# Kernel optimization log

Hardware: AMD Instinct MI355X
Metric: run time of the kernel (lower is better)

## Reference

```python
import jax, jax.numpy as jnp
import numpy as np

EPS_RMS = 1e-6
EPS_Q = 1e-5


def _weight_quant(w):
    # BitNet b1.58-style ternary weight quantization with mean-abs scale
    scale = 1.0 / jnp.clip(jnp.mean(jnp.abs(w)), EPS_Q)
    wq = jnp.clip(jnp.round(w * scale), -1.0, 1.0) / scale
    return w + jax.lax.stop_gradient(wq - w)  # STE


def _activation_quant(x):
    # per-token 8-bit absmax quantization
    scale = 127.0 / jnp.clip(jnp.max(jnp.abs(x), axis=-1, keepdims=True), EPS_Q)
    xq = jnp.clip(jnp.round(x * scale), -128.0, 127.0) / scale
    return x + jax.lax.stop_gradient(xq - x)  # STE


def _rmsnorm(x, weight):
    inv = jax.lax.rsqrt(jnp.mean(x * x, axis=-1, keepdims=True) + EPS_RMS)
    return x * inv * weight


def setup_inputs() -> dict:
    key = jax.random.key(0)
    k1, k2, k3 = jax.random.split(key, 3)
    B, S, D, CD = 8, 4096, 1024, 1024
    x = jax.random.normal(k1, (B, S, D), dtype=jnp.float32)
    c = jax.random.normal(k2, (B, CD), dtype=jnp.float32)
    # NOTE: the module zero-inits proj; we use small random weights so the
    # quantized conditioning path is numerically exercised.
    w_proj = jax.random.normal(k3, (2 * D, CD), dtype=jnp.float32) * 0.02
    b_proj = jnp.zeros((2 * D,), dtype=jnp.float32)
    rms_weight = jnp.ones((D,), dtype=jnp.float32)
    return {"x": x, "c": c, "w_proj": w_proj, "b_proj": b_proj, "rms_weight": rms_weight}


def reference(x, c, w_proj, b_proj, rms_weight):
    if c.ndim == 2:
        c = c[:, None, :]  # [B, 1, cond_dim]
    # BitLinear: quantized activations x quantized ternary weights
    cq = _activation_quant(c)
    wq = _weight_quant(w_proj)
    emb = jnp.einsum('btc,dc->btd', cq, wq) + b_proj  # [B, 1, 2*dim]
    scale, shift = jnp.split(emb, 2, axis=-1)
    xn = _rmsnorm(x, rms_weight)
    return xn * (1.0 + scale) + shift
```

## Files before the change

### kernel.cpp

```cpp
#include <hip/hip_runtime.h>
#include <math.h>


constexpr int Bn = 8;
constexpr int Sn = 4096;
constexpr int Dn = 1024;
constexpr int TWO_D = 2048;
constexpr int OFF_PART = 0;
constexpr int OFF_CQ   = 4096;
constexpr int OFF_SC   = 16384;
constexpr int OFF_SH   = 24576;

__device__ __forceinline__ float waveReduceSumBcast(float v) {
#pragma unroll
    for (int off = 32; off > 0; off >>= 1) v += __shfl_xor(v, off, 64);
    return v;
}
__device__ __forceinline__ float waveReduceMaxBcast(float v) {
#pragma unroll
    for (int off = 32; off > 0; off >>= 1) v = fmaxf(v, __shfl_xor(v, off, 64));
    return v;
}

__global__ void k_pre(const float* __restrict__ w, const float* __restrict__ c,
                      float* __restrict__ part, float* __restrict__ cq) {
    int tid = threadIdx.x;
    if (blockIdx.x < TWO_D) {
        size_t base = (size_t)blockIdx.x * 1024 + (size_t)tid * 4;
        float4 v = *(const float4*)(w + base);
        float s = fabsf(v.x) + fabsf(v.y) + fabsf(v.z) + fabsf(v.w);
        s = waveReduceSumBcast(s);
        __shared__ float lds[4];
        if ((tid & 63) == 0) lds[tid >> 6] = s;
        __syncthreads();
        if (tid == 0) part[blockIdx.x] = lds[0] + lds[1] + lds[2] + lds[3];
    } else {
        int b = blockIdx.x - TWO_D;
        float4 v = ((const float4*)(c + (size_t)b * Dn))[tid];
        float m = fmaxf(fmaxf(fabsf(v.x), fabsf(v.y)), fmaxf(fabsf(v.z), fabsf(v.w)));
        m = waveReduceMaxBcast(m);
        __shared__ float lm[4];
        if ((tid & 63) == 0) lm[tid >> 6] = m;
        __syncthreads();
        float mx = fmaxf(fmaxf(lm[0], lm[1]), fmaxf(lm[2], lm[3]));
        float scale = 127.0f / fmaxf(mx, 1e-5f);
        float inv = 1.0f / scale;
        float4 q;
        q.x = fminf(fmaxf(rintf(v.x * scale), -128.0f), 127.0f) * inv;
        q.y = fminf(fmaxf(rintf(v.y * scale), -128.0f), 127.0f) * inv;
        q.z = fminf(fmaxf(rintf(v.z * scale), -128.0f), 127.0f) * inv;
        q.w = fminf(fmaxf(rintf(v.w * scale), -128.0f), 127.0f) * inv;
        ((float4*)(cq + (size_t)b * Dn))[tid] = q;
    }
}

__global__ void k_emb(const float* __restrict__ w, const float* __restrict__ bp,
                      const float* __restrict__ cq, const float* __restrict__ part,
                      float* __restrict__ sc, float* __restrict__ sh) {
    int tid = threadIdx.x;
    float s = 0.0f;
#pragma unroll
    for (int k = 0; k < 8; ++k) s += part[tid + k * 256];
    s = waveReduceSumBcast(s);
    __shared__ float lds[4];
    if ((tid & 63) == 0) lds[tid >> 6] = s;
    __syncthreads();
    float mw = fmaxf((lds[0] + lds[1] + lds[2] + lds[3]) * (1.0f / 2097152.0f), 1e-5f);
    float sw = 1.0f / mw;

    int lane = tid & 63;
    int d = (blockIdx.x * blockDim.x + tid) >> 6;
    const float* wr = w + (size_t)d * 1024 + (size_t)lane * 16;
    float t[16];
#pragma unroll
    for (int j = 0; j < 16; j += 4) {
        float4 v = *(const float4*)(wr + j);
        t[j + 0] = fminf(fmaxf(rintf(v.x * sw), -1.0f), 1.0f);
        t[j + 1] = fminf(fmaxf(rintf(v.y * sw), -1.0f), 1.0f);
        t[j + 2] = fminf(fmaxf(rintf(v.z * sw), -1.0f), 1.0f);
        t[j + 3] = fminf(fmaxf(rintf(v.w * sw), -1.0f), 1.0f);
    }
    for (int b = 0; b < Bn; ++b) {
        const float* cr = cq + (size_t)b * 1024 + (size_t)lane * 16;
        float dot = 0.0f;
#pragma unroll
        for (int j = 0; j < 16; j += 4) {
            float4 u = *(const float4*)(cr + j);
            dot += t[j + 0] * u.x + t[j + 1] * u.y + t[j + 2] * u.z + t[j + 3] * u.w;
        }
        dot = waveReduceSumBcast(dot);
        if (lane == 0) {
            float val = dot * mw + bp[d];
            if (d < Dn) sc[b * Dn + d] = 1.0f + val;
            else        sh[b * Dn + (d - Dn)] = val;
        }
    }
}

__global__ void __launch_bounds__(256) k_main(
        const float* __restrict__ x, const float* __restrict__ rw,
        const float* __restrict__ sc, const float* __restrict__ sh,
        float* __restrict__ out) {
    int tid  = threadIdx.x;
    int lane = tid & 63;
    int row  = blockIdx.x * 4 + (tid >> 6);
    int b    = row >> 12;

    const float4* xr = (const float4*)(x + (size_t)row * Dn);
    float4 v0 = xr[lane];
    float4 v1 = xr[lane + 64];
    float4 v2 = xr[lane + 128];
    float4 v3 = xr[lane + 192];

    float ss = v0.x*v0.x + v0.y*v0.y + v0.z*v0.z + v0.w*v0.w
             + v1.x*v1.x + v1.y*v1.y + v1.z*v1.z + v1.w*v1.w
             + v2.x*v2.x + v2.y*v2.y + v2.z*v2.z + v2.w*v2.w
             + v3.x*v3.x + v3.y*v3.y + v3.z*v3.z + v3.w*v3.w;
    ss = waveReduceSumBcast(ss);
    float inv = rsqrtf(ss * (1.0f / 1024.0f) + 1e-6f);

    const float4* rwv = (const float4*)rw;
    const float4* s1v = (const float4*)(sc + (size_t)b * Dn);
    const float4* s0v = (const float4*)(sh + (size_t)b * Dn);
    float4* ov = (float4*)(out + (size_t)row * Dn);

#pragma unroll
    for (int q = 0; q < 4; ++q) {
        int idx = lane + q * 64;
        float4 v = (q == 0) ? v0 : (q == 1) ? v1 : (q == 2) ? v2 : v3;
        float4 wv = rwv[idx];
        float4 s1 = s1v[idx];
        float4 s0 = s0v[idx];
        float4 o;
        o.x = v.x * inv * wv.x * s1.x + s0.x;
        o.y = v.y * inv * wv.y * s1.y + s0.y;
        o.z = v.z * inv * wv.z * s1.z + s0.z;
        o.w = v.w * inv * wv.w * s1.w + s0.w;
        ov[idx] = o;
    }
}

extern "C" void kernel_launch(void* const* d_in, const int* in_sizes, int n_in,
                              void* d_out, int out_size, void* d_ws, size_t ws_size,
                              hipStream_t stream) {
    const float* x  = (const float*)d_in[0];
    const float* c  = (const float*)d_in[1];
    const float* w  = (const float*)d_in[2];
    const float* bp = (const float*)d_in[3];
    const float* rw = (const float*)d_in[4];
    float* out = (float*)d_out;
    float* ws  = (float*)d_ws;

    float* part = ws + OFF_PART;
    float* cq   = ws + OFF_CQ;
    float* sc   = ws + OFF_SC;
    float* sh   = ws + OFF_SH;

    k_pre <<<TWO_D + Bn, 256, 0, stream>>>(w, c, part, cq);
    k_emb <<<TWO_D / 4, 256, 0, stream>>>(w, bp, cq, part, sc, sh);
    k_main<<<Bn * Sn / 4, 256, 0, stream>>>(x, rw, sc, sh, out);
}
```

Before: 63.30 us.

## Fold RMS weight into scale, prefetch rows with nontemporal loads in main kernel

Precomputes g = rms_weight*(1+scale) in the embedding kernel so the main kernel reads one fewer vector per element. The main kernel now launches fewer blocks, each processing four rows with the next row's data prefetched via nontemporal loads to overlap memory latency. The embedding kernel also batches wave reductions across all batches. Fewer blocks may reduce occupancy-based latency hiding.

```diff
diff --git a/kernel.cpp b/kernel.cpp
--- a/kernel.cpp
+++ b/kernel.cpp
@@ -8,8 +8,10 @@
 constexpr int TWO_D = 2048;
 constexpr int OFF_PART = 0;
 constexpr int OFF_CQ   = 4096;
-constexpr int OFF_SC   = 16384;
+constexpr int OFF_G    = 16384;
 constexpr int OFF_SH   = 24576;
+
+using f4 = __attribute__((ext_vector_type(4))) float;
 
 __device__ __forceinline__ float waveReduceSumBcast(float v) {
 #pragma unroll
@@ -27,7 +29,7 @@
     int tid = threadIdx.x;
     if (blockIdx.x < TWO_D) {
         size_t base = (size_t)blockIdx.x * 1024 + (size_t)tid * 4;
-        float4 v = *(const float4*)(w + base);
+        f4 v = *(const f4*)(w + base);
         float s = fabsf(v.x) + fabsf(v.y) + fabsf(v.z) + fabsf(v.w);
         s = waveReduceSumBcast(s);
         __shared__ float lds[4];
@@ -36,7 +38,7 @@
         if (tid == 0) part[blockIdx.x] = lds[0] + lds[1] + lds[2] + lds[3];
     } else {
         int b = blockIdx.x - TWO_D;
-        float4 v = ((const float4*)(c + (size_t)b * Dn))[tid];
+        f4 v = ((const f4*)(c + (size_t)b * Dn))[tid];
         float m = fmaxf(fmaxf(fabsf(v.x), fabsf(v.y)), fmaxf(fabsf(v.z), fabsf(v.w)));
         m = waveReduceMaxBcast(m);
         __shared__ float lm[4];
@@ -45,18 +47,19 @@
         float mx = fmaxf(fmaxf(lm[0], lm[1]), fmaxf(lm[2], lm[3]));
         float scale = 127.0f / fmaxf(mx, 1e-5f);
         float inv = 1.0f / scale;
-        float4 q;
+        f4 q;
         q.x = fminf(fmaxf(rintf(v.x * scale), -128.0f), 127.0f) * inv;
         q.y = fminf(fmaxf(rintf(v.y * scale), -128.0f), 127.0f) * inv;
         q.z = fminf(fmaxf(rintf(v.z * scale), -128.0f), 127.0f) * inv;
         q.w = fminf(fmaxf(rintf(v.w * scale), -128.0f), 127.0f) * inv;
-        ((float4*)(cq + (size_t)b * Dn))[tid] = q;
+        ((f4*)(cq + (size_t)b * Dn))[tid] = q;
     }
 }
 
 __global__ void k_emb(const float* __restrict__ w, const float* __restrict__ bp,
                       const float* __restrict__ cq, const float* __restrict__ part,
-                      float* __restrict__ sc, float* __restrict__ sh) {
+                      const float* __restrict__ rw,
+                      float* __restrict__ g, float* __restrict__ sh) {
     int tid = threadIdx.x;
     float s = 0.0f;
 #pragma unroll
@@ -74,69 +77,94 @@
     float t[16];
 #pragma unroll
     for (int j = 0; j < 16; j += 4) {
-        float4 v = *(const float4*)(wr + j);
+        f4 v = *(const f4*)(wr + j);
         t[j + 0] = fminf(fmaxf(rintf(v.x * sw), -1.0f), 1.0f);
         t[j + 1] = fminf(fmaxf(rintf(v.y * sw), -1.0f), 1.0f);
         t[j + 2] = fminf(fmaxf(rintf(v.z * sw), -1.0f), 1.0f);
         t[j + 3] = fminf(fmaxf(rintf(v.w * sw), -1.0f), 1.0f);
     }
+    float acc[Bn];
+#pragma unroll
     for (int b = 0; b < Bn; ++b) {
-        const float* cr = cq + (size_t)b * 1024 + (size_t)lane * 16;
+        const float* cr = cq + (size_t)b * Dn + (size_t)lane * 16;
         float dot = 0.0f;
 #pragma unroll
         for (int j = 0; j < 16; j += 4) {
-            float4 u = *(const float4*)(cr + j);
+            f4 u = *(const f4*)(cr + j);
             dot += t[j + 0] * u.x + t[j + 1] * u.y + t[j + 2] * u.z + t[j + 3] * u.w;
         }
-        dot = waveReduceSumBcast(dot);
-        if (lane == 0) {
-            float val = dot * mw + bp[d];
-            if (d < Dn) sc[b * Dn + d] = 1.0f + val;
-            else        sh[b * Dn + (d - Dn)] = val;
+        acc[b] = dot;
+    }
+#pragma unroll
+    for (int off = 32; off > 0; off >>= 1) {
+#pragma unroll
+        for (int b = 0; b < Bn; ++b) acc[b] += __shfl_xor(acc[b], off, 64);
+    }
+    if (lane == 0) {
+        float bias = bp[d];
+        if (d < Dn) {
+            float rwd = rw[d];
+#pragma unroll
+            for (int b = 0; b < Bn; ++b)
+                g[b * Dn + d] = rwd * (1.0f + (acc[b] * mw + bias));
+        } else {
+#pragma unroll
+            for (int b = 0; b < Bn; ++b)
+                sh[b * Dn + (d - Dn)] = acc[b] * mw + bias;
         }
     }
 }
 
 __global__ void __launch_bounds__(256) k_main(
-        const float* __restrict__ x, const float* __restrict__ rw,
-        const float* __restrict__ sc, const float* __restrict__ sh,
-        float* __restrict__ out) {
+        const float* __restrict__ x, const float* __restrict__ g,
+        const float* __restrict__ sh, float* __restrict__ out) {
+    constexpr int NW = 2048 * 4;
     int tid  = threadIdx.x;
     int lane = tid & 63;
     int row  = blockIdx.x * 4 + (tid >> 6);
-    int b    = row >> 12;
 
-    const float4* xr = (const float4*)(x + (size_t)row * Dn);
-    float4 v0 = xr[lane];
-    float4 v1 = xr[lane + 64];
-    float4 v2 = xr[lane + 128];
-    float4 v3 = xr[lane + 192];
-
-    float ss = v0.x*v0.x + v0.y*v0.y + v0.z*v0.z + v0.w*v0.w
-             + v1.x*v1.x + v1.y*v1.y + v1.z*v1.z + v1.w*v1.w
-             + v2.x*v2.x + v2.y*v2.y + v2.z*v2.z + v2.w*v2.w
-             + v3.x*v3.x + v3.y*v3.y + v3.z*v3.z + v3.w*v3.w;
-    ss = waveReduceSumBcast(ss);
-    float inv = rsqrtf(ss * (1.0f / 1024.0f) + 1e-6f);
-
-    const float4* rwv = (const float4*)rw;
-    const float4* s1v = (const float4*)(sc + (size_t)b * Dn);
-    const float4* s0v = (const float4*)(sh + (size_t)b * Dn);
-    float4* ov = (float4*)(out + (size_t)row * Dn);
+    const f4* xr = (const f4*)(x + (size_t)row * Dn);
+    f4 v0 = __builtin_nontemporal_load(&xr[lane]);
+    f4 v1 = __builtin_nontemporal_load(&xr[lane + 64]);
+    f4 v2 = __builtin_nontemporal_load(&xr[lane + 128]);
+    f4 v3 = __builtin_nontemporal_load(&xr[lane + 192]);
 
 #pragma unroll
-    for (int q = 0; q < 4; ++q) {
-        int idx = lane + q * 64;
-        float4 v = (q == 0) ? v0 : (q == 1) ? v1 : (q == 2) ? v2 : v3;
-        float4 wv = rwv[idx];
-        float4 s1 = s1v[idx];
-        float4 s0 = s0v[idx];
-        float4 o;
-        o.x = v.x * inv * wv.x * s1.x + s0.x;
-        o.y = v.y * inv * wv.y * s1.y + s0.y;
-        o.z = v.z * inv * wv.z * s1.z + s0.z;
-        o.w = v.w * inv * wv.w * s1.w + s0.w;
-        ov[idx] = o;
+    for (int it = 0; it < 4; ++it) {
+        int nrow = row + NW;
+        f4 n0, n1, n2, n3;
+        if (it < 3) {
+            const f4* xn = (const f4*)(x + (size_t)nrow * Dn);
+            n0 = __builtin_nontemporal_load(&xn[lane]);
+            n1 = __builtin_nontemporal_load(&xn[lane + 64]);
+            n2 = __builtin_nontemporal_load(&xn[lane + 128]);
+            n3 = __builtin_nontemporal_load(&xn[lane + 192]);
+        }
+        float ss = v0.x*v0.x + v0.y*v0.y + v0.z*v0.z + v0.w*v0.w
+                 + v1.x*v1.x + v1.y*v1.y + v1.z*v1.z + v1.w*v1.w
+                 + v2.x*v2.x + v2.y*v2.y + v2.z*v2.z + v2.w*v2.w
+                 + v3.x*v3.x + v3.y*v3.y + v3.z*v3.z + v3.w*v3.w;
+        ss = waveReduceSumBcast(ss);
+        float inv = rsqrtf(ss * (1.0f / 1024.0f) + 1e-6f);
+
+        int b = row >> 12;
+        const f4* gv  = (const f4*)(g  + (size_t)b * Dn);
+        const f4* s0v = (const f4*)(sh + (size_t)b * Dn);
+        f4* ov = (f4*)(out + (size_t)row * Dn);
+#pragma unroll
+        for (int q = 0; q < 4; ++q) {
+            int idx = lane + q * 64;
+            f4 v = (q == 0) ? v0 : (q == 1) ? v1 : (q == 2) ? v2 : v3;
+            f4 gg = gv[idx];
+            f4 s0 = s0v[idx];
+            f4 o;
+            o.x = v.x * inv * gg.x + s0.x;
+            o.y = v.y * inv * gg.y + s0.y;
+            o.z = v.z * inv * gg.z + s0.z;
+            o.w = v.w * inv * gg.w + s0.w;
+            ov[idx] = o;
+        }
+        if (it < 3) { v0 = n0; v1 = n1; v2 = n2; v3 = n3; row = nrow; }
     }
 }
 
@@ -153,10 +181,10 @@
 
     float* part = ws + OFF_PART;
     float* cq   = ws + OFF_CQ;
-    float* sc   = ws + OFF_SC;
+    float* g    = ws + OFF_G;
     float* sh   = ws + OFF_SH;
 
     k_pre <<<TWO_D + Bn, 256, 0, stream>>>(w, c, part, cq);
-    k_emb <<<TWO_D / 4, 256, 0, stream>>>(w, bp, cq, part, sc, sh);
-    k_main<<<Bn * Sn / 4, 256, 0, stream>>>(x, rw, sc, sh, out);
+    k_emb <<<TWO_D / 4, 256, 0, stream>>>(w, bp, cq, part, rw, g, sh);
+    k_main<<<TWO_D, 256, 0, stream>>>(x, g, sh, out);
 }
```

Result: slower. 64.66 us (+2.2%).
